# Optimization experiments

Hardware: AMD Instinct MI355X
Metric: run time of the kernel (lower is better)

The kernel has to match this reference:

```python
import jax, jax.numpy as jnp
import numpy as np
from jax import lax

N = 8192          # instances
B1 = 256          # first-level bags (32 instances each)
B2 = 16           # second-level bags (16 first-level bags each)
FLAT = 5 * 5 * 64 # flatten dim after conv/pool stack
UNITS = 512


def _conv_relu(x, w, b):
    # x: NHWC, w: HWIO, VALID conv + relu (Keras Conv2D default)
    y = lax.conv_general_dilated(x, w, (1, 1), 'VALID',
                                 dimension_numbers=('NHWC', 'HWIO', 'NHWC'))
    return jax.nn.relu(y + b)


def _maxpool2(x):
    return lax.reduce_window(x, -jnp.inf, lax.max,
                             (1, 2, 2, 1), (1, 2, 2, 1), 'VALID')


def _segment_mean(e, ids, num_segments):
    # e: [M, D], ids: [M] sorted segment ids covering 0..num_segments-1
    s = jax.ops.segment_sum(e, ids, num_segments=num_segments)
    c = jax.ops.segment_sum(jnp.ones((e.shape[0], 1), e.dtype), ids,
                            num_segments=num_segments)
    return s / c


def setup_inputs() -> dict:
    key = jax.random.key(0)
    ks = jax.random.split(key, 8)
    x = jax.random.normal(ks[0], (N, 28, 28, 1), dtype=jnp.float32)
    # contiguous equal-size bags, matching the contiguous gather_nd runs
    first_lab = (jnp.arange(N, dtype=jnp.int32) // (N // B1))
    second_lab = (jnp.arange(B1, dtype=jnp.int32) // (B1 // B2))
    conv1_w = jax.random.normal(ks[1], (3, 3, 1, 32), dtype=jnp.float32) * 0.1
    conv1_b = jnp.zeros((32,), jnp.float32)
    conv2_w = jax.random.normal(ks[2], (3, 3, 32, 64), dtype=jnp.float32) * 0.05
    conv2_b = jnp.zeros((64,), jnp.float32)
    fc1_w = jax.random.normal(ks[3], (FLAT, UNITS), dtype=jnp.float32) * 0.02
    fc1_b = jnp.zeros((UNITS,), jnp.float32)
    fc2_w = jax.random.normal(ks[4], (UNITS, 1), dtype=jnp.float32) * 0.05
    fc2_b = jnp.zeros((1,), jnp.float32)
    return {'x': x, 'conv1_w': conv1_w, 'conv1_b': conv1_b,
            'conv2_w': conv2_w, 'conv2_b': conv2_b,
            'fc1_w': fc1_w, 'fc1_b': fc1_b, 'fc2_w': fc2_w, 'fc2_b': fc2_b,
            'first_lab': first_lab, 'second_lab': second_lab}


def reference(x, conv1_w, conv1_b, conv2_w, conv2_b,
              fc1_w, fc1_b, fc2_w, fc2_b, first_lab, second_lab):
    h = _conv_relu(x, conv1_w, conv1_b)        # [N,26,26,32]
    h = _maxpool2(h)                            # [N,13,13,32]
    h = _conv_relu(h, conv2_w, conv2_b)         # [N,11,11,64]
    h = _maxpool2(h)                            # [N,5,5,64]
    first_emb = h.reshape(h.shape[0], -1)       # [N,1600]
    second_emb = _segment_mean(first_emb, first_lab, B1)   # [B1,1600]
    third_emb = _segment_mean(second_emb, second_lab, B2)  # [B2,1600]
    outer = jnp.max(third_emb, axis=0, keepdims=True)      # [1,1600]
    pred = outer @ fc1_w + fc1_b                # Dense (linear), dropout is
    pred = pred                                  # identity at inference
    pred = jax.nn.sigmoid(pred @ fc2_w + fc2_b)  # [1,1]
    return pred
```

## Files before the change

kernel.cpp:

```cpp
#include <hip/hip_runtime.h>
#include <hip/hip_bf16.h>
#include <math.h>

#define N_IMG 8192
#define GROUPS 16
#define EMB 1600
#define IPB 8

typedef __attribute__((ext_vector_type(8))) short short8;
typedef __attribute__((ext_vector_type(16))) float f32x16;
typedef __attribute__((ext_vector_type(4))) unsigned int u32x4;
typedef __attribute__((ext_vector_type(8))) unsigned int u32x8;
typedef __attribute__((ext_vector_type(8))) int i32x8;

#define WS_W2F8 102400
#define WS_W1F  122880
#define WS_V    123904

__device__ __forceinline__ unsigned short bfc(float f) {
    return __builtin_bit_cast(unsigned short, __float2bfloat16(f));
}
__device__ __forceinline__ unsigned pk2(float a, float b) {
    return (unsigned)bfc(a) | ((unsigned)bfc(b) << 16);
}
__device__ __forceinline__ unsigned char f2fp8(float f) {
    return (unsigned char)(__builtin_amdgcn_cvt_pk_fp8_f32(f, f, 0, false) & 0xFF);
}

__global__ __launch_bounds__(256) void prep(
        const float* __restrict__ w1, const float* __restrict__ w2,
        const float* __restrict__ fc1w, const float* __restrict__ fc2w,
        float* __restrict__ gsum, unsigned short* __restrict__ w1f,
        unsigned char* __restrict__ w2f8, float* __restrict__ v)
{
    int gid = blockIdx.x * 256 + threadIdx.x;
    if (gid < 25600) { gsum[gid] = 0.f; return; }
    gid -= 25600;
    if (gid < 20480) {
        int u = gid & 31, n = (gid >> 5) & 63, t = gid >> 11;
        unsigned char q = 0;
        if (t < 9) q = f2fp8(w2[(t * 32 + u) * 64 + n]);
        w2f8[gid] = q;
        return;
    }
    gid -= 20480;
    if (gid < 512) {
        int j = gid & 7, ll = gid >> 3;
        int k = 8 * (ll >> 5) + j;
        int r = k >> 2, c4 = k & 3, co = ll & 31;
        w1f[gid] = (r < 3 && c4 < 3) ? bfc(w1[(r * 3 + c4) * 32 + co])
                                     : (unsigned short)0;
        return;
    }
    gid -= 512;
    if (gid < 1600) {
        const float4* a = (const float4*)(fc1w + gid * 512);
        const float4* bq = (const float4*)fc2w;
        float s = 0.f;
        for (int q = 0; q < 128; ++q) {
            float4 av = a[q], bv = bq[q];
            s += av.x * bv.x + av.y * bv.y + av.z * bv.z + av.w * bv.w;
        }
        v[gid] = s;
    }
}

__global__ __launch_bounds__(256) void fused(
        const float* __restrict__ x,
        const unsigned short* __restrict__ w1f, const float* __restrict__ b1,
        const unsigned char* __restrict__ w2f8, const float* __restrict__ b2,
        float* __restrict__ gsum)
{
    __shared__ __align__(16) unsigned short simgb[2 * 1568];
    __shared__ __align__(16) unsigned char sp2[2 * 6912];

    const int tid = threadIdx.x;
    const int wv = tid >> 6;
    const int l = tid & 63;
    const int l31 = l & 31, lh = l >> 5;
    const int mw = wv & 1, nw = wv >> 1;

    const short8 wb1 = *(const short8*)(w1f + l * 8);
    const float cb1 = b1[l31];

    i32x8 bb[5];
    #pragma unroll
    for (int c = 0; c < 5; ++c)
        bb[c] = *(const i32x8*)(w2f8 + ((2 * c + lh) * 64 + 32 * nw + l31) * 32);
    const float cb2 = b2[32 * nw + l31];

    const int rb_inv = 2 * ((l & 1) * 784 + ((l >> 1) & 1) * 28 + 56 * lh);
    const int wb_inv = 384 * wv + 48 * lh + l31;
    const int ew = 8 * wv + (l31 >> 2);
    int posq0, posq1;
    {
        int m2 = 32 * mw + l31;
        int q2i = m2 >> 2, idx2 = m2 & 3;
        posq0 = ((2 * (q2i / 5) + (idx2 >> 1)) * 12 + 2 * (q2i % 5) + (idx2 & 1)) * 48;
        m2 = 32 * (2 + mw) + l31; if (m2 > 99) m2 = 99;
        q2i = m2 >> 2; idx2 = m2 & 3;
        posq1 = ((2 * (q2i / 5) + (idx2 >> 1)) * 12 + 2 * (q2i % 5) + (idx2 & 1)) * 48;
    }
    const int o0 = lh ? 48   : 0;
    const int o1 = lh ? 576  : 96;
    const int o2 = lh ? 672  : 624;
    const int o3 = lh ? 1200 : 1152;
    const int o4 = lh ? 0    : 1248;

    float pacc[2][4];
    #pragma unroll
    for (int a = 0; a < 2; ++a)
        #pragma unroll
        for (int b = 0; b < 4; ++b) pacc[a][b] = 0.f;

    const int imgbase = blockIdx.x * IPB;
    const float* xbase = x + (size_t)imgbase * 784;

    if (tid < 98) {
        const float4* xg = (const float4*)xbase;
        float4 A = xg[2 * tid], B = xg[2 * tid + 1];
        float sc = xbase[(8 * tid + 8 < 784) ? 8 * tid + 8 : 783];
        *(u32x4*)(&simgb[8 * tid]) =
            (u32x4){pk2(A.x, A.y), pk2(A.z, A.w), pk2(B.x, B.y), pk2(B.z, B.w)};
        *(u32x4*)(&simgb[784 + 8 * tid]) =
            (u32x4){pk2(A.y, A.z), pk2(A.w, B.x), pk2(B.y, B.z), pk2(B.w, sc)};
    }
    asm volatile("s_waitcnt lgkmcnt(0)" ::: "memory");
    __builtin_amdgcn_s_barrier();

    for (int ii = 0; ii < IPB; ++ii) {
        const int SOFF = (ii & 1) * 3136;
        const int POFF = (ii & 1) * 6912;
        const char* rb = (const char*)simgb + (SOFF + rb_inv);
        unsigned char* wb = sp2 + (POFF + wb_inv);

        float4 A4, B4; float sc = 0.f;
        const bool pf = (ii + 1 < IPB) && (tid < 98);
        if (pf) {
            const float4* xn = (const float4*)(xbase + (ii + 1) * 784);
            A4 = xn[2 * tid]; B4 = xn[2 * tid + 1];
            sc = xbase[(ii + 1) * 784 + ((8 * tid + 8 < 784) ? 8 * tid + 8 : 783)];
        }

        #pragma unroll
        for (int t9 = 0; t9 < 5; ++t9) {
            if (4 * t9 + wv < 18) {
                const int qd = 32 * t9 + ew;
                const int pr = qd / 12, pc = qd - 12 * pr;
                const unsigned* bp = (const unsigned*)(rb + (112 * pr + 4 * pc));
                const unsigned d0 = bp[0], d1 = bp[1], d2 = bp[14], d3 = bp[15];
                const short8 af = __builtin_bit_cast(short8, (u32x4){d0, d1, d2, d3});
                f32x16 cc;
                #pragma unroll
                for (int z = 0; z < 16; ++z) cc[z] = cb1;
                cc = __builtin_amdgcn_mfma_f32_32x32x16_bf16(af, wb1, cc, 0, 0, 0);
                #pragma unroll
                for (int rq = 0; rq < 4; ++rq) {
                    float p = fmaxf(fmaxf(fmaxf(fmaxf(cc[4 * rq], cc[4 * rq + 1]),
                                                cc[4 * rq + 2]), cc[4 * rq + 3]), 0.f);
                    wb[1536 * t9 + 96 * rq] = f2fp8(p);
                }
            }
        }

        if (pf) {
            unsigned short* dst = (unsigned short*)((char*)simgb + (SOFF ^ 3136));
            *(u32x4*)(&dst[8 * tid]) =
                (u32x4){pk2(A4.x, A4.y), pk2(A4.z, A4.w), pk2(B4.x, B4.y), pk2(B4.z, B4.w)};
            *(u32x4*)(&dst[784 + 8 * tid]) =
                (u32x4){pk2(A4.y, A4.z), pk2(A4.w, B4.x), pk2(B4.y, B4.z), pk2(B4.w, sc)};
        }
        asm volatile("s_waitcnt lgkmcnt(0)" ::: "memory");
        __builtin_amdgcn_s_barrier();

        #pragma unroll
        for (int mti = 0; mti < 2; ++mti) {
            const unsigned char* ab = sp2 + POFF + (mti ? posq1 : posq0);
            f32x16 acc;
            #pragma unroll
            for (int z = 0; z < 16; ++z) acc[z] = cb2;
#define C2STEP(OC, CI)                                                          \
            {                                                                   \
                u32x4 r0 = *(const u32x4*)(ab + (OC));                          \
                u32x4 r1 = *(const u32x4*)(ab + (OC) + 16);                     \
                i32x8 af8 = __builtin_bit_cast(i32x8,                           \
                    __builtin_shufflevector(r0, r1, 0, 1, 2, 3, 4, 5, 6, 7));   \
                acc = __builtin_amdgcn_mfma_scale_f32_32x32x64_f8f6f4(          \
                    af8, bb[CI], acc, 0, 0, 0, 127, 0, 127);                    \
            }
            C2STEP(o0, 0)
            C2STEP(o1, 1)
            C2STEP(o2, 2)
            C2STEP(o3, 3)
            C2STEP(o4, 4)
#undef C2STEP
            #pragma unroll
            for (int rq = 0; rq < 4; ++rq) {
                float p = fmaxf(fmaxf(fmaxf(fmaxf(acc[4 * rq], acc[4 * rq + 1]),
                                            acc[4 * rq + 2]), acc[4 * rq + 3]), 0.f);
                pacc[mti][rq] += p;
            }
        }
    }

    const int grp = imgbase >> 9;
    float* gs = gsum + grp * EMB;
    #pragma unroll
    for (int mti = 0; mti < 2; ++mti) {
        const int mt = 2 * mti + mw;
        #pragma unroll
        for (int rq = 0; rq < 4; ++rq) {
            if (mt < 3 || (rq == 0 && lh == 0)) {
                const int q2 = 8 * mt + 2 * rq + lh;
                atomicAdd(&gs[q2 * 64 + 32 * nw + l31], pacc[mti][rq]);
            }
        }
    }
}

__global__ __launch_bounds__(256) void head(
        const float* __restrict__ gsum, const float* __restrict__ v,
        const float* __restrict__ fc1b, const float* __restrict__ fc2w,
        const float* __restrict__ fc2b, float* __restrict__ out)
{
    __shared__ float sred[256];
    const int tid = threadIdx.x;
    float partial = 0.f;
    const float4* g4 = (const float4*)gsum;
    const float4* v4 = (const float4*)v;
    for (int i = tid; i < 400; i += 256) {
        float4 m = g4[i];
        #pragma unroll
        for (int gg = 1; gg < GROUPS; ++gg) {
            float4 t = g4[gg * 400 + i];
            m.x = fmaxf(m.x, t.x); m.y = fmaxf(m.y, t.y);
            m.z = fmaxf(m.z, t.z); m.w = fmaxf(m.w, t.w);
        }
        float4 vv = v4[i];
        partial += m.x * vv.x + m.y * vv.y + m.z * vv.z + m.w * vv.w;
    }
    partial *= (1.f / 512.f);
    partial += fc1b[tid] * fc2w[tid] + fc1b[tid + 256] * fc2w[tid + 256];
    sred[tid] = partial;
    __syncthreads();
    for (int s = 128; s > 0; s >>= 1) {
        if (tid < s) sred[tid] += sred[tid + s];
        __syncthreads();
    }
    if (tid == 0) out[0] = 1.f / (1.f + expf(-(sred[0] + fc2b[0])));
}

extern "C" void kernel_launch(void* const* d_in, const int* in_sizes, int n_in,
                              void* d_out, int out_size, void* d_ws, size_t ws_size,
                              hipStream_t stream)
{
    const float* x    = (const float*)d_in[0];
    const float* w1   = (const float*)d_in[1];
    const float* b1   = (const float*)d_in[2];
    const float* w2   = (const float*)d_in[3];
    const float* b2   = (const float*)d_in[4];
    const float* fc1w = (const float*)d_in[5];
    const float* fc1b = (const float*)d_in[6];
    const float* fc2w = (const float*)d_in[7];
    const float* fc2b = (const float*)d_in[8];

    float* gsum = (float*)d_ws;
    unsigned char* w2f8 = (unsigned char*)d_ws + WS_W2F8;
    unsigned short* w1f = (unsigned short*)((char*)d_ws + WS_W1F);
    float* v = (float*)((char*)d_ws + WS_V);

    prep<<<189, 256, 0, stream>>>(w1, w2, fc1w, fc2w, gsum, w1f, w2f8, v);
    fused<<<N_IMG / IPB, 256, 0, stream>>>(x, w1f, b1, w2f8, b2, gsum);
    head<<<1, 256, 0, stream>>>(gsum, v, fc1b, fc2w, fc2b, (float*)d_out);
}
```

Before: 58.54 us.

## Reassign conv2 MFMA tiles per wave, stream FP8 weights, parallelize fc fold

Each wave in the conv2 stage now owns one M tile and computes both 32-channel N halves with two accumulators, instead of two M tiles for one N half. The FP8 weight fragments are loaded from global memory (cache) inside the MFMA loop rather than held in registers for the whole kernel, and launch_bounds asks for 4 blocks per CU. This lowers register pressure to raise occupancy, but adds repeated weight loads in the hot loop. The prep kernel's fc1·fc2 dot products now use one wavefront per row with a shuffle reduction, which needs a larger grid.

```diff
diff --git a/kernel.cpp b/kernel.cpp
--- a/kernel.cpp
+++ b/kernel.cpp
@@ -10,7 +10,6 @@
 typedef __attribute__((ext_vector_type(8))) short short8;
 typedef __attribute__((ext_vector_type(16))) float f32x16;
 typedef __attribute__((ext_vector_type(4))) unsigned int u32x4;
-typedef __attribute__((ext_vector_type(8))) unsigned int u32x8;
 typedef __attribute__((ext_vector_type(8))) int i32x8;
 
 #define WS_W2F8 102400
@@ -35,37 +34,40 @@
 {
     int gid = blockIdx.x * 256 + threadIdx.x;
     if (gid < 25600) { gsum[gid] = 0.f; return; }
-    gid -= 25600;
-    if (gid < 20480) {
-        int u = gid & 31, n = (gid >> 5) & 63, t = gid >> 11;
+    if (gid < 46080) {
+        int i = gid - 25600;
+        int u = i & 31, n = (i >> 5) & 63, t = i >> 11;
         unsigned char q = 0;
         if (t < 9) q = f2fp8(w2[(t * 32 + u) * 64 + n]);
-        w2f8[gid] = q;
+        w2f8[i] = q;
         return;
     }
-    gid -= 20480;
-    if (gid < 512) {
-        int j = gid & 7, ll = gid >> 3;
+    if (gid < 46592) {
+        int i = gid - 46080;
+        int j = i & 7, ll = i >> 3;
         int k = 8 * (ll >> 5) + j;
         int r = k >> 2, c4 = k & 3, co = ll & 31;
-        w1f[gid] = (r < 3 && c4 < 3) ? bfc(w1[(r * 3 + c4) * 32 + co])
-                                     : (unsigned short)0;
+        w1f[i] = (r < 3 && c4 < 3) ? bfc(w1[(r * 3 + c4) * 32 + co])
+                                   : (unsigned short)0;
         return;
     }
-    gid -= 512;
-    if (gid < 1600) {
-        const float4* a = (const float4*)(fc1w + gid * 512);
-        const float4* bq = (const float4*)fc2w;
-        float s = 0.f;
-        for (int q = 0; q < 128; ++q) {
-            float4 av = a[q], bv = bq[q];
-            s += av.x * bv.x + av.y * bv.y + av.z * bv.z + av.w * bv.w;
-        }
-        v[gid] = s;
-    }
-}
-
-__global__ __launch_bounds__(256) void fused(
+    {
+        const int d = (gid - 46592) >> 6;
+        if (d < 1600) {
+            const int lane = gid & 63;
+            const float4* a = (const float4*)(fc1w + d * 512 + lane * 8);
+            const float4* b = (const float4*)(fc2w + lane * 8);
+            const float4 a0 = a[0], a1 = a[1], b0 = b[0], b1 = b[1];
+            float s = a0.x * b0.x + a0.y * b0.y + a0.z * b0.z + a0.w * b0.w
+                    + a1.x * b1.x + a1.y * b1.y + a1.z * b1.z + a1.w * b1.w;
+            #pragma unroll
+            for (int off = 32; off; off >>= 1) s += __shfl_xor(s, off);
+            if (lane == 0) v[d] = s;
+        }
+    }
+}
+
+__global__ __launch_bounds__(256, 4) void fused(
         const float* __restrict__ x,
         const unsigned short* __restrict__ w1f, const float* __restrict__ b1,
         const unsigned char* __restrict__ w2f8, const float* __restrict__ b2,
@@ -78,28 +80,21 @@
     const int wv = tid >> 6;
     const int l = tid & 63;
     const int l31 = l & 31, lh = l >> 5;
-    const int mw = wv & 1, nw = wv >> 1;
 
     const short8 wb1 = *(const short8*)(w1f + l * 8);
     const float cb1 = b1[l31];
 
-    i32x8 bb[5];
-    #pragma unroll
-    for (int c = 0; c < 5; ++c)
-        bb[c] = *(const i32x8*)(w2f8 + ((2 * c + lh) * 64 + 32 * nw + l31) * 32);
-    const float cb2 = b2[32 * nw + l31];
+    const int bgo = 2048 * lh + 32 * l31;
+    const float cb20 = b2[l31], cb21 = b2[32 + l31];
 
     const int rb_inv = 2 * ((l & 1) * 784 + ((l >> 1) & 1) * 28 + 56 * lh);
     const int wb_inv = 384 * wv + 48 * lh + l31;
     const int ew = 8 * wv + (l31 >> 2);
-    int posq0, posq1;
+    int posq;
     {
-        int m2 = 32 * mw + l31;
-        int q2i = m2 >> 2, idx2 = m2 & 3;
-        posq0 = ((2 * (q2i / 5) + (idx2 >> 1)) * 12 + 2 * (q2i % 5) + (idx2 & 1)) * 48;
-        m2 = 32 * (2 + mw) + l31; if (m2 > 99) m2 = 99;
-        q2i = m2 >> 2; idx2 = m2 & 3;
-        posq1 = ((2 * (q2i / 5) + (idx2 >> 1)) * 12 + 2 * (q2i % 5) + (idx2 & 1)) * 48;
+        int m2 = 32 * wv + l31; if (m2 > 99) m2 = 99;
+        const int q2i = m2 >> 2, idx2 = m2 & 3;
+        posq = ((2 * (q2i / 5) + (idx2 >> 1)) * 12 + 2 * (q2i % 5) + (idx2 & 1)) * 48;
     }
     const int o0 = lh ? 48   : 0;
     const int o1 = lh ? 576  : 96;
@@ -107,11 +102,8 @@
     const int o3 = lh ? 1200 : 1152;
     const int o4 = lh ? 0    : 1248;
 
-    float pacc[2][4];
-    #pragma unroll
-    for (int a = 0; a < 2; ++a)
-        #pragma unroll
-        for (int b = 0; b < 4; ++b) pacc[a][b] = 0.f;
+    float pacc0[4] = {0.f, 0.f, 0.f, 0.f};
+    float pacc1[4] = {0.f, 0.f, 0.f, 0.f};
 
     const int imgbase = blockIdx.x * IPB;
     const float* xbase = x + (size_t)imgbase * 784;
@@ -173,20 +165,23 @@
         asm volatile("s_waitcnt lgkmcnt(0)" ::: "memory");
         __builtin_amdgcn_s_barrier();
 
-        #pragma unroll
-        for (int mti = 0; mti < 2; ++mti) {
-            const unsigned char* ab = sp2 + POFF + (mti ? posq1 : posq0);
-            f32x16 acc;
+        {
+            const unsigned char* ab = sp2 + POFF + posq;
+            f32x16 acc0, acc1;
             #pragma unroll
-            for (int z = 0; z < 16; ++z) acc[z] = cb2;
+            for (int z = 0; z < 16; ++z) { acc0[z] = cb20; acc1[z] = cb21; }
 #define C2STEP(OC, CI)                                                          \
             {                                                                   \
+                const i32x8 bf0 = *(const i32x8*)(w2f8 + bgo + 4096 * (CI));    \
+                const i32x8 bf1 = *(const i32x8*)(w2f8 + bgo + 4096 * (CI) + 1024); \
                 u32x4 r0 = *(const u32x4*)(ab + (OC));                          \
                 u32x4 r1 = *(const u32x4*)(ab + (OC) + 16);                     \
                 i32x8 af8 = __builtin_bit_cast(i32x8,                           \
                     __builtin_shufflevector(r0, r1, 0, 1, 2, 3, 4, 5, 6, 7));   \
-                acc = __builtin_amdgcn_mfma_scale_f32_32x32x64_f8f6f4(          \
-                    af8, bb[CI], acc, 0, 0, 0, 127, 0, 127);                    \
+                acc0 = __builtin_amdgcn_mfma_scale_f32_32x32x64_f8f6f4(         \
+                    af8, bf0, acc0, 0, 0, 0, 127, 0, 127);                      \
+                acc1 = __builtin_amdgcn_mfma_scale_f32_32x32x64_f8f6f4(         \
+                    af8, bf1, acc1, 0, 0, 0, 127, 0, 127);                      \
             }
             C2STEP(o0, 0)
             C2STEP(o1, 1)
@@ -196,9 +191,12 @@
 #undef C2STEP
             #pragma unroll
             for (int rq = 0; rq < 4; ++rq) {
-                float p = fmaxf(fmaxf(fmaxf(fmaxf(acc[4 * rq], acc[4 * rq + 1]),
-                                            acc[4 * rq + 2]), acc[4 * rq + 3]), 0.f);
-                pacc[mti][rq] += p;
+                float p0 = fmaxf(fmaxf(fmaxf(fmaxf(acc0[4 * rq], acc0[4 * rq + 1]),
+                                             acc0[4 * rq + 2]), acc0[4 * rq + 3]), 0.f);
+                float p1 = fmaxf(fmaxf(fmaxf(fmaxf(acc1[4 * rq], acc1[4 * rq + 1]),
+                                             acc1[4 * rq + 2]), acc1[4 * rq + 3]), 0.f);
+                pacc0[rq] += p0;
+                pacc1[rq] += p1;
             }
         }
     }
@@ -206,14 +204,11 @@
     const int grp = imgbase >> 9;
     float* gs = gsum + grp * EMB;
     #pragma unroll
-    for (int mti = 0; mti < 2; ++mti) {
-        const int mt = 2 * mti + mw;
-        #pragma unroll
-        for (int rq = 0; rq < 4; ++rq) {
-            if (mt < 3 || (rq == 0 && lh == 0)) {
-                const int q2 = 8 * mt + 2 * rq + lh;
-                atomicAdd(&gs[q2 * 64 + 32 * nw + l31], pacc[mti][rq]);
-            }
+    for (int rq = 0; rq < 4; ++rq) {
+        if (wv < 3 || (rq == 0 && lh == 0)) {
+            const int q2 = 8 * wv + 2 * rq + lh;
+            atomicAdd(&gs[q2 * 64 + l31],      pacc0[rq]);
+            atomicAdd(&gs[q2 * 64 + 32 + l31], pacc1[rq]);
         }
     }
 }
@@ -269,7 +264,7 @@
     unsigned short* w1f = (unsigned short*)((char*)d_ws + WS_W1F);
     float* v = (float*)((char*)d_ws + WS_V);
 
-    prep<<<189, 256, 0, stream>>>(w1, w2, fc1w, fc2w, gsum, w1f, w2f8, v);
+    prep<<<582, 256, 0, stream>>>(w1, w2, fc1w, fc2w, gsum, w1f, w2f8, v);
     fused<<<N_IMG / IPB, 256, 0, stream>>>(x, w1f, b1, w2f8, b2, gsum);
     head<<<1, 256, 0, stream>>>(gsum, v, fc1b, fc2w, fc2b, (float*)d_out);
 }
```

After: 102.1 us. 1.74x slower.
